# Performance work log

Hardware: AMD Instinct MI355X
Metric: run time of the kernel (lower is better)

The kernel has to match this reference:

```python
import jax, jax.numpy as jnp
import numpy as np


def setup_inputs() -> dict:
    key = jax.random.key(0)
    k1, k2 = jax.random.split(key)
    B, N, C, H, W = 64, 8, 256, 4, 4
    pred = jax.random.normal(k1, (B, N, C, H, W), dtype=jnp.float32)
    gt = jax.random.normal(k2, (B, N, C, H, W), dtype=jnp.float32)
    return {"pred": pred, "gt": gt}


def reference(pred, gt):
    B, N, C, H, W = pred.shape
    M = B * N * H * W
    # pred.permute(0,1,3,4,2).reshape(M, C)
    p = jnp.transpose(pred, (0, 1, 3, 4, 2)).reshape(M, C)
    # gt.permute(2,0,1,3,4).reshape(C, M)
    g = jnp.transpose(gt, (2, 0, 1, 3, 4)).reshape(C, M)
    logits = p @ g  # (M, M)
    # CrossEntropyLoss with targets = arange(M): mean of (logsumexep(row) - diag)
    lse = jax.nn.logsumexp(logits, axis=1)
    diag = jnp.diagonal(logits)
    loss = jnp.mean(lse - diag)
    return loss
```

## Files before the change

### kernel.cpp

```cpp
#include <hip/hip_runtime.h>
#include <hip/hip_bf16.h>
#include <stdint.h>

typedef int   i32x4  __attribute__((ext_vector_type(4)));
typedef int   v8i    __attribute__((ext_vector_type(8)));
typedef float f32x4  __attribute__((ext_vector_type(4)));
typedef float f32x16 __attribute__((ext_vector_type(16)));

#define LOG2E   1.4426950408889634f
#define LN2     0.6931471805599453f
#define C_SCALED 86.56170245f
#define SCALE1  0x7F7F7F7F

__device__ __forceinline__ void gload_lds16(const void* gsrc, void* ldst) {
    __builtin_amdgcn_global_load_lds(
        (const __attribute__((address_space(1))) unsigned int*)gsrc,
        (__attribute__((address_space(3))) unsigned int*)ldst,
        16, 0, 0);
}

__global__ void convert_perm(const float* __restrict__ pred, const float* __restrict__ gt,
                             unsigned char* __restrict__ Ab, unsigned char* __restrict__ Bb,
                             unsigned int* __restrict__ counter)
{
    if (blockIdx.x == 0 && threadIdx.x == 0) *counter = 0u;
    const int slab = blockIdx.x & 511;
    const bool isA = blockIdx.x < 512;
    const float scale = isA ? LOG2E : 1.0f;
    const float* src = (isA ? pred : gt) + (size_t)slab * 4096;
    unsigned char* dst = (isA ? Ab : Bb) + (size_t)slab * 4096;
    const int t  = threadIdx.x;
    const int hw = t >> 4;
    const int c0 = (t & 15) * 16;
    int d[4];
    #pragma unroll
    for (int q = 0; q < 4; ++q) {
        const float v0 = src[(c0 + q * 4 + 0) * 16 + hw] * scale;
        const float v1 = src[(c0 + q * 4 + 1) * 16 + hw] * scale;
        const float v2 = src[(c0 + q * 4 + 2) * 16 + hw] * scale;
        const float v3 = src[(c0 + q * 4 + 3) * 16 + hw] * scale;
        int r = __builtin_amdgcn_cvt_pk_fp8_f32(v0, v1, 0, false);
        r     = __builtin_amdgcn_cvt_pk_fp8_f32(v2, v3, r, true);
        d[q] = r;
    }
    *(i32x4*)(dst + hw * 256 + c0) = (i32x4){d[0], d[1], d[2], d[3]};
}

__global__ __launch_bounds__(128) __attribute__((amdgpu_waves_per_eu(2, 2)))
void gemm_lse(const unsigned char* __restrict__ Ab, const unsigned char* __restrict__ Bb,
              float* __restrict__ rowsum_part, float* __restrict__ diagy)
{
    __shared__ __align__(16) char lds[32768];
    const int tid  = threadIdx.x;
    const int lane = tid & 63;
    const int w    = tid >> 6;
    const int l31  = lane & 31;
    const int hi   = lane >> 5;

    const int jc = blockIdx.x & 15;
    const int ib = blockIdx.x >> 4;
    const int i0 = ib << 7;
    const int j0 = jc << 9;

    v8i pfr[2][4];
    {
        const unsigned char* base = Ab + (size_t)(i0 + w * 64 + l31) * 256 + hi * 32;
        #pragma unroll
        for (int f = 0; f < 2; ++f)
            #pragma unroll
            for (int ks = 0; ks < 4; ++ks)
                pfr[f][ks] = *(const v8i*)(base + f * 32 * 256 + ks * 64);
    }

    const unsigned char* Bbase = Bb + (size_t)j0 * 256;
    const int ibase = i0 + w * 64;

#define STG_ALL(NSRC, NBUF) { \
    _Pragma("unroll") \
    for (int it_ = 0; it_ < 8; ++it_) { \
        const int ob_ = it_ * 2048 + tid * 16; \
        const int sb_ = ob_ ^ (((ob_ >> 8) & 15) << 4); \
        gload_lds16((NSRC) + sb_, (NBUF) + ob_); \
    } }

    STG_ALL(Bbase, lds);

    float rs[2] = {0.f, 0.f};

#define READB(G, JF) { \
    const char* rp_ = lds + (js & 1) * 16384 + ((JF) * 32 + l31) * 256; \
    const int sx_ = (((JF) * 32 + l31) & 15) << 4; \
    _Pragma("unroll") \
    for (int ks_ = 0; ks_ < 4; ++ks_) { \
        const int ko_ = ks_ * 64 + hi * 32; \
        const i32x4 lo_ = *(const i32x4*)(rp_ + ((ko_     ) ^ sx_)); \
        const i32x4 h_  = *(const i32x4*)(rp_ + ((ko_ + 16) ^ sx_)); \
        G[ks_] = (v8i){lo_[0], lo_[1], lo_[2], lo_[3], h_[0], h_[1], h_[2], h_[3]}; \
    } }

#define MMJ(G, A0, A1) { \
    __builtin_amdgcn_s_setprio(1); \
    _Pragma("unroll") \
    for (int ks_ = 0; ks_ < 4; ++ks_) { \
        A0 = __builtin_amdgcn_mfma_scale_f32_32x32x64_f8f6f4( \
            G[ks_], pfr[0][ks_], A0, 0, 0, 0, SCALE1, 0, SCALE1); \
        A1 = __builtin_amdgcn_mfma_scale_f32_32x32x64_f8f6f4( \
            G[ks_], pfr[1][ks_], A1, 0, 0, 0, SCALE1, 0, SCALE1); \
    } \
    __builtin_amdgcn_s_setprio(0); }

#define ZA16(X) { _Pragma("unroll") for (int r_ = 0; r_ < 16; ++r_) X[r_] = -C_SCALED; }

#define EPJ(ACC, IFR, JF) { \
    const int jb_  = jbase + (JF) * 32; \
    const int ibf_ = ibase + (IFR) * 32; \
    float e_[16]; \
    _Pragma("unroll") for (int r_ = 0; r_ < 16; ++r_) e_[r_] = __builtin_amdgcn_exp2f(ACC[r_]); \
    float s_ = ((e_[0]+e_[1])+(e_[2]+e_[3])) + ((e_[4]+e_[5])+(e_[6]+e_[7])) \
             + ((e_[8]+e_[9])+(e_[10]+e_[11])) + ((e_[12]+e_[13])+(e_[14]+e_[15])); \
    if (ibf_ == jb_) { \
        _Pragma("unroll") \
        for (int r_ = 0; r_ < 16; ++r_) \
            if (((r_ & 3) + 8 * (r_ >> 2) + 4 * hi) == l31) diagy[ibf_ + l31] = ACC[r_]; \
    } \
    rs[IFR] += s_; }

    for (int js = 0; js < 8; ++js) {
        asm volatile("s_waitcnt vmcnt(0)" ::: "memory");
        __builtin_amdgcn_s_barrier();

        char*                nbuf  = lds + ((js + 1) & 1) * 16384;
        const unsigned char* nsrc  = Bbase + (size_t)(js + 1) * 16384;
        const int            jbase = j0 + js * 64;

        v8i g0[4], g1[4];
        f32x16 a00, a10, a01, a11;

        READB(g0, 0);
        if (js < 7) STG_ALL(nsrc, nbuf);
        READB(g1, 1);

        ZA16(a00); ZA16(a10);
        MMJ(g0, a00, a10);
        EPJ(a00, 0, 0); EPJ(a10, 1, 0);

        ZA16(a01); ZA16(a11);
        MMJ(g1, a01, a11);
        EPJ(a01, 0, 1); EPJ(a11, 1, 1);
    }

#undef STG_ALL
#undef READB
#undef MMJ
#undef ZA16
#undef EPJ

    #pragma unroll
    for (int f = 0; f < 2; ++f) {
        float v = rs[f];
        v += __shfl_xor(v, 32);
        if (lane < 32)
            rowsum_part[(size_t)(i0 + w * 64 + f * 32 + lane) * 16 + jc] = v;
    }
}

__global__ __launch_bounds__(1024) void reduce_partial(const float* __restrict__ rowsum_part,
                                                       const float* __restrict__ diagy,
                                                       float* __restrict__ accum,
                                                       unsigned int* __restrict__ counter,
                                                       float* __restrict__ out)
{
    const int i = blockIdx.x * 1024 + threadIdx.x;
    const f32x4* p = (const f32x4*)(rowsum_part + (size_t)i * 16);
    float s = 0.f;
    #pragma unroll
    for (int k = 0; k < 4; ++k) {
        const f32x4 v = p[k];
        s += (v[0] + v[1]) + (v[2] + v[3]);
    }
    float val = __log2f(s) - diagy[i];
    #pragma unroll
    for (int d = 1; d < 64; d <<= 1) val += __shfl_xor(val, d);
    __shared__ float red[16];
    if ((threadIdx.x & 63) == 0) red[threadIdx.x >> 6] = val;
    __syncthreads();
    if (threadIdx.x == 0) {
        float t = 0.f;
        #pragma unroll
        for (int k = 0; k < 16; ++k) t += red[k];
        accum[blockIdx.x] = t;
        __threadfence();
        const unsigned n = atomicAdd(counter, 1u);
        if (n == 7u) {
            float tt = 0.f;
            const volatile float* av = (const volatile float*)accum;
            #pragma unroll
            for (int k = 0; k < 8; ++k) tt += av[k];
            out[0] = LN2 * tt * (1.0f / 8192.0f);
        }
    }
}

extern "C" void kernel_launch(void* const* d_in, const int* in_sizes, int n_in,
                              void* d_out, int out_size, void* d_ws, size_t ws_size,
                              hipStream_t stream) {
    const float* pred = (const float*)d_in[0];
    const float* gt   = (const float*)d_in[1];
    float* out = (float*)d_out;

    char* ws = (char*)d_ws;
    float*         accum       = (float*)(ws);
    unsigned int*  counter     = (unsigned int*)(ws + 0x100);
    float*         diagy       = (float*)(ws + 0x1000);
    float*         rowsum_part = (float*)(ws + 0x10000);
    unsigned char* Ab          = (unsigned char*)(ws + 0x100000);
    unsigned char* Bb          = (unsigned char*)(ws + 0x300000);

    convert_perm<<<1024, 256, 0, stream>>>(pred, gt, Ab, Bb, counter);
    gemm_lse<<<1024, 128, 0, stream>>>(Ab, Bb, rowsum_part, diagy);
    reduce_partial<<<8, 1024, 0, stream>>>(rowsum_part, diagy, accum, counter, out);
}
```

Before: 40.79 us.

## Drop LDS staging in GEMM-LSE; load B fragments directly from global per wave

Result: slower. 55.48 us (+36.0%).

```diff
diff --git a/kernel.cpp b/kernel.cpp
--- a/kernel.cpp
+++ b/kernel.cpp
@@ -11,13 +11,6 @@
 #define LN2     0.6931471805599453f
 #define C_SCALED 86.56170245f
 #define SCALE1  0x7F7F7F7F
-
-__device__ __forceinline__ void gload_lds16(const void* gsrc, void* ldst) {
-    __builtin_amdgcn_global_load_lds(
-        (const __attribute__((address_space(1))) unsigned int*)gsrc,
-        (__attribute__((address_space(3))) unsigned int*)ldst,
-        16, 0, 0);
-}
 
 __global__ void convert_perm(const float* __restrict__ pred, const float* __restrict__ gt,
                              unsigned char* __restrict__ Ab, unsigned char* __restrict__ Bb,
@@ -46,25 +39,22 @@
     *(i32x4*)(dst + hw * 256 + c0) = (i32x4){d[0], d[1], d[2], d[3]};
 }
 
-__global__ __launch_bounds__(128) __attribute__((amdgpu_waves_per_eu(2, 2)))
+__global__ __launch_bounds__(64) __attribute__((amdgpu_waves_per_eu(2, 2)))
 void gemm_lse(const unsigned char* __restrict__ Ab, const unsigned char* __restrict__ Bb,
               float* __restrict__ rowsum_part, float* __restrict__ diagy)
 {
-    __shared__ __align__(16) char lds[32768];
-    const int tid  = threadIdx.x;
-    const int lane = tid & 63;
-    const int w    = tid >> 6;
+    const int lane = threadIdx.x & 63;
     const int l31  = lane & 31;
     const int hi   = lane >> 5;
 
     const int jc = blockIdx.x & 15;
     const int ib = blockIdx.x >> 4;
-    const int i0 = ib << 7;
+    const int i0 = ib << 6;
     const int j0 = jc << 9;
 
     v8i pfr[2][4];
     {
-        const unsigned char* base = Ab + (size_t)(i0 + w * 64 + l31) * 256 + hi * 32;
+        const unsigned char* base = Ab + (size_t)(i0 + l31) * 256 + hi * 32;
         #pragma unroll
         for (int f = 0; f < 2; ++f)
             #pragma unroll
@@ -73,28 +63,16 @@
     }
 
     const unsigned char* Bbase = Bb + (size_t)j0 * 256;
-    const int ibase = i0 + w * 64;
-
-#define STG_ALL(NSRC, NBUF) { \
-    _Pragma("unroll") \
-    for (int it_ = 0; it_ < 8; ++it_) { \
-        const int ob_ = it_ * 2048 + tid * 16; \
-        const int sb_ = ob_ ^ (((ob_ >> 8) & 15) << 4); \
-        gload_lds16((NSRC) + sb_, (NBUF) + ob_); \
-    } }
-
-    STG_ALL(Bbase, lds);
+    const int ibase = i0;
 
     float rs[2] = {0.f, 0.f};
 
-#define READB(G, JF) { \
-    const char* rp_ = lds + (js & 1) * 16384 + ((JF) * 32 + l31) * 256; \
-    const int sx_ = (((JF) * 32 + l31) & 15) << 4; \
+#define LOADB(G, JS, JF) { \
+    const unsigned char* rp_ = Bbase + (size_t)((JS) * 64 + (JF) * 32 + l31) * 256 + hi * 32; \
     _Pragma("unroll") \
     for (int ks_ = 0; ks_ < 4; ++ks_) { \
-        const int ko_ = ks_ * 64 + hi * 32; \
-        const i32x4 lo_ = *(const i32x4*)(rp_ + ((ko_     ) ^ sx_)); \
-        const i32x4 h_  = *(const i32x4*)(rp_ + ((ko_ + 16) ^ sx_)); \
+        const i32x4 lo_ = *(const i32x4*)(rp_ + ks_ * 64); \
+        const i32x4 h_  = *(const i32x4*)(rp_ + ks_ * 64 + 16); \
         G[ks_] = (v8i){lo_[0], lo_[1], lo_[2], lo_[3], h_[0], h_[1], h_[2], h_[3]}; \
     } }
 
@@ -111,46 +89,39 @@
 
 #define ZA16(X) { _Pragma("unroll") for (int r_ = 0; r_ < 16; ++r_) X[r_] = -C_SCALED; }
 
-#define EPJ(ACC, IFR, JF) { \
-    const int jb_  = jbase + (JF) * 32; \
+#define EPJ(ACC, IFR, JB) { \
     const int ibf_ = ibase + (IFR) * 32; \
     float e_[16]; \
     _Pragma("unroll") for (int r_ = 0; r_ < 16; ++r_) e_[r_] = __builtin_amdgcn_exp2f(ACC[r_]); \
     float s_ = ((e_[0]+e_[1])+(e_[2]+e_[3])) + ((e_[4]+e_[5])+(e_[6]+e_[7])) \
              + ((e_[8]+e_[9])+(e_[10]+e_[11])) + ((e_[12]+e_[13])+(e_[14]+e_[15])); \
-    if (ibf_ == jb_) { \
+    if (ibf_ == (JB)) { \
         _Pragma("unroll") \
         for (int r_ = 0; r_ < 16; ++r_) \
             if (((r_ & 3) + 8 * (r_ >> 2) + 4 * hi) == l31) diagy[ibf_ + l31] = ACC[r_]; \
     } \
     rs[IFR] += s_; }
 
+    v8i g0[4], g1[4];
+    LOADB(g0, 0, 0);
+    LOADB(g1, 0, 1);
+
     for (int js = 0; js < 8; ++js) {
-        asm volatile("s_waitcnt vmcnt(0)" ::: "memory");
-        __builtin_amdgcn_s_barrier();
+        const int jbase = j0 + js * 64;
+        f32x16 a0, a1;
 
-        char*                nbuf  = lds + ((js + 1) & 1) * 16384;
-        const unsigned char* nsrc  = Bbase + (size_t)(js + 1) * 16384;
-        const int            jbase = j0 + js * 64;
+        ZA16(a0); ZA16(a1);
+        MMJ(g0, a0, a1);
+        EPJ(a0, 0, jbase); EPJ(a1, 1, jbase);
+        if (js < 7) LOADB(g0, js + 1, 0);
 
-        v8i g0[4], g1[4];
-        f32x16 a00, a10, a01, a11;
-
-        READB(g0, 0);
-        if (js < 7) STG_ALL(nsrc, nbuf);
-        READB(g1, 1);
-
-        ZA16(a00); ZA16(a10);
-        MMJ(g0, a00, a10);
-        EPJ(a00, 0, 0); EPJ(a10, 1, 0);
-
-        ZA16(a01); ZA16(a11);
-        MMJ(g1, a01, a11);
-        EPJ(a01, 0, 1); EPJ(a11, 1, 1);
+        ZA16(a0); ZA16(a1);
+        MMJ(g1, a0, a1);
+        EPJ(a0, 0, jbase + 32); EPJ(a1, 1, jbase + 32);
+        if (js < 7) LOADB(g1, js + 1, 1);
     }
 
-#undef STG_ALL
-#undef READB
+#undef LOADB
 #undef MMJ
 #undef ZA16
 #undef EPJ
@@ -160,7 +131,7 @@
         float v = rs[f];
         v += __shfl_xor(v, 32);
         if (lane < 32)
-            rowsum_part[(size_t)(i0 + w * 64 + f * 32 + lane) * 16 + jc] = v;
+            rowsum_part[(size_t)(i0 + f * 32 + lane) * 16 + jc] = v;
     }
 }
 
@@ -217,6 +188,6 @@
     unsigned char* Bb          = (unsigned char*)(ws + 0x300000);
 
     convert_perm<<<1024, 256, 0, stream>>>(pred, gt, Ab, Bb, counter);
-    gemm_lse<<<1024, 128, 0, stream>>>(Ab, Bb, rowsum_part, diagy);
+    gemm_lse<<<2048, 64, 0, stream>>>(Ab, Bb, rowsum_part, diagy);
     reduce_partial<<<8, 1024, 0, stream>>>(rowsum_part, diagy, accum, counter, out);
 }
```
